# Kernel tuning notes

Measured on AMD Instinct MI355X. Metric: run time of the kernel, lower is better.

The kernel has to match this reference:

```python
import jax, jax.numpy as jnp
import numpy as np

THRESH = 1.0   # firing threshold used in forward1 (IF_Neuron(..., 1.0))
EPS = 1e-5     # spike detection epsilon from SpikingNN
T_NORM = 256.0 # hard-coded divisor in forward1
GAMMA = 1.0 / 2.2

# SpikingNN: forward is a hard 0/1 spike, backward is a straight-through
# pass gated on ex_membrane > EPS (matches the torch autograd.Function).
@jax.custom_vjp
def spike(ex):
    return (ex > EPS).astype(ex.dtype)

def _spike_fwd(ex):
    return (ex > EPS).astype(ex.dtype), (ex > EPS)

def _spike_bwd(mask, g):
    return (jnp.where(mask, g, 0.0),)

spike.defvjp(_spike_fwd, _spike_bwd)

def _sif_forward(x):
    # x: [T, H, W, C]; sequential IF-neuron integrate/fire scan over T.
    def step(mem, xt):
        mem = mem + xt
        # torch F.threshold(mem, thr, 0): mem where mem > thr else 0;
        # its grad passes only where mem > thr (jnp.where matches this).
        ex = jnp.where(mem > THRESH, mem, jnp.zeros_like(mem))
        mem = mem - ex  # soft reset: subtract the excess membrane
        s = spike(ex)
        # out = s.detach() + (1/thr)*s - (1/thr)*s.detach()
        # value == s; grad w.r.t. s scaled by 1/thr (straight-through trick)
        sg = jax.lax.stop_gradient(s)
        out = sg + (1.0 / THRESH) * s - (1.0 / THRESH) * sg
        return mem, out

    mem0 = jnp.zeros(x.shape[1:], dtype=x.dtype)
    _, outs = jax.lax.scan(step, mem0, x)  # outs: [T, H, W, C]
    y = jnp.sum(outs, axis=0) / T_NORM
    return y ** GAMMA  # gamma correction, pow(y, 1/2.2)

def setup_inputs() -> dict:
    key = jax.random.key(0)
    # uniform [0,1) spike-camera-like intensities so the IF neuron fires
    x = jax.random.uniform(key, (256, 256, 256, 3), dtype=jnp.float32)
    return {"x": x}

def reference(x):
    return _sif_forward(x)
```

## Files before the change

### kernel.cpp

```cpp
#include <hip/hip_runtime.h>
#include <math.h>


#define T_STEPS 256
#define NPIX (256 * 256 * 3)

__global__ __launch_bounds__(256) void sif_kernel(const float* __restrict__ x,
                                                  float* __restrict__ out) {
    const int pix = blockIdx.x * blockDim.x + threadIdx.x;
    if (pix >= NPIX) return;

    const float* __restrict__ p = x + pix;

    float mem = 0.0f;
    float cnt = 0.0f;

#pragma unroll 8
    for (int t = 0; t < T_STEPS; ++t) {
        const float v = p[(size_t)t * NPIX];
        mem += v;
        const bool fire = mem > 1.0f;
        cnt += fire ? 1.0f : 0.0f;
        mem  = fire ? 0.0f : mem;
    }

    const float y = cnt * (1.0f / 256.0f);
    out[pix] = powf(y, 1.0f / 2.2f);
}

extern "C" void kernel_launch(void* const* d_in, const int* in_sizes, int n_in,
                              void* d_out, int out_size, void* d_ws, size_t ws_size,
                              hipStream_t stream) {
    const float* x = (const float*)d_in[0];
    float* out = (float*)d_out;

    const int threads = 256;
    const int blocks = NPIX / threads;
    sif_kernel<<<blocks, threads, 0, stream>>>(x, out);
}
```

Baseline: 263.2 us.

## Vectorize time scan with float4 loads and double-buffered register prefetch

Each thread now processes four adjacent pixels with float4 loads and keeps two register buffers of eight time steps. It issues the next batch of loads before integrating the current one. This aims to raise memory-level parallelism and cut load instruction count for a bandwidth-bound scan. In exchange, the thread count drops fourfold and blocks shrink to 64 threads, which lowers occupancy and raises register pressure.

```diff
diff --git a/kernel.cpp b/kernel.cpp
--- a/kernel.cpp
+++ b/kernel.cpp
@@ -4,28 +4,50 @@
 
 #define T_STEPS 256
 #define NPIX (256 * 256 * 3)
+#define NV (NPIX / 4)
+#define PF 8
 
-__global__ __launch_bounds__(256) void sif_kernel(const float* __restrict__ x,
-                                                  float* __restrict__ out) {
-    const int pix = blockIdx.x * blockDim.x + threadIdx.x;
-    if (pix >= NPIX) return;
+__device__ __forceinline__ void sif_step(float4& mem, float4& cnt, float4 v) {
+    mem.x += v.x; mem.y += v.y; mem.z += v.z; mem.w += v.w;
+    bool fx = mem.x > 1.0f, fy = mem.y > 1.0f, fz = mem.z > 1.0f, fw = mem.w > 1.0f;
+    cnt.x += fx ? 1.0f : 0.0f; cnt.y += fy ? 1.0f : 0.0f;
+    cnt.z += fz ? 1.0f : 0.0f; cnt.w += fw ? 1.0f : 0.0f;
+    mem.x = fx ? 0.0f : mem.x; mem.y = fy ? 0.0f : mem.y;
+    mem.z = fz ? 0.0f : mem.z; mem.w = fw ? 0.0f : mem.w;
+}
 
-    const float* __restrict__ p = x + pix;
+__global__ __launch_bounds__(64) void sif_kernel(const float* __restrict__ x,
+                                                 float* __restrict__ out) {
+    const int gid = blockIdx.x * blockDim.x + threadIdx.x;
+    const float4* __restrict__ p = reinterpret_cast<const float4*>(x) + gid;
 
-    float mem = 0.0f;
-    float cnt = 0.0f;
+    float4 mem = make_float4(0.f, 0.f, 0.f, 0.f);
+    float4 cnt = make_float4(0.f, 0.f, 0.f, 0.f);
 
-#pragma unroll 8
-    for (int t = 0; t < T_STEPS; ++t) {
-        const float v = p[(size_t)t * NPIX];
-        mem += v;
-        const bool fire = mem > 1.0f;
-        cnt += fire ? 1.0f : 0.0f;
-        mem  = fire ? 0.0f : mem;
+    float4 a[PF], b[PF];
+
+#pragma unroll
+    for (int k = 0; k < PF; ++k) a[k] = p[k * NV];
+
+    for (int tb = 0; tb < T_STEPS / PF; ++tb) {
+        if (tb + 1 < T_STEPS / PF) {
+            const int base = (tb + 1) * PF;
+#pragma unroll
+            for (int k = 0; k < PF; ++k) b[k] = p[(base + k) * NV];
+        }
+#pragma unroll
+        for (int k = 0; k < PF; ++k) sif_step(mem, cnt, a[k]);
+#pragma unroll
+        for (int k = 0; k < PF; ++k) a[k] = b[k];
     }
 
-    const float y = cnt * (1.0f / 256.0f);
-    out[pix] = powf(y, 1.0f / 2.2f);
+    const float g = 1.0f / 2.2f;
+    float4 r;
+    r.x = powf(cnt.x * (1.0f / 256.0f), g);
+    r.y = powf(cnt.y * (1.0f / 256.0f), g);
+    r.z = powf(cnt.z * (1.0f / 256.0f), g);
+    r.w = powf(cnt.w * (1.0f / 256.0f), g);
+    reinterpret_cast<float4*>(out)[gid] = r;
 }
 
 extern "C" void kernel_launch(void* const* d_in, const int* in_sizes, int n_in,
@@ -34,7 +56,7 @@
     const float* x = (const float*)d_in[0];
     float* out = (float*)d_out;
 
-    const int threads = 256;
-    const int blocks = NPIX / threads;
+    const int threads = 64;
+    const int blocks = NV / threads;
     sif_kernel<<<blocks, threads, 0, stream>>>(x, out);
 }
```

After: 261.9 us. Within noise of the previous version (-0.5%).
